# Kernel tuning notes

Hardware: AMD Instinct MI355X
Metric: run time of the kernel (lower is better)

Reference implementation:

```python
import jax, jax.numpy as jnp
import numpy as np

N_USERS, N_MOVIES, N_EDGES = 100000, 20000, 1000000
IN_UNITS, NUM_CLASSES = 128, 5


def _xavier(key, shape):
    # torch xavier_uniform_ on a Linear weight [out, in]; we store transposed [in, out]
    fan_in, fan_out = shape[0], shape[1]
    a = jnp.sqrt(6.0 / (fan_in + fan_out))
    return jax.random.uniform(key, shape, dtype=jnp.float32, minval=-a, maxval=a)


def setup_inputs() -> dict:
    key = jax.random.key(0)
    k1, k2, k3, k4, k5, k6, k7 = jax.random.split(key, 7)
    ufeat = jax.random.normal(k1, (N_USERS, IN_UNITS), dtype=jnp.float32)
    ifeat = jax.random.normal(k2, (N_MOVIES, IN_UNITS), dtype=jnp.float32)
    src_idx = jax.random.randint(k3, (N_EDGES,), 0, N_USERS, dtype=jnp.int32)
    dst_idx = jax.random.randint(k4, (N_EDGES,), 0, N_MOVIES, dtype=jnp.int32)
    W1 = _xavier(k5, (2 * IN_UNITS, IN_UNITS))   # Linear(2*in_units -> in_units)
    W2 = _xavier(k6, (IN_UNITS, IN_UNITS))       # Linear(in_units -> in_units)
    Wp = _xavier(k7, (IN_UNITS, NUM_CLASSES))    # predictor Linear(in_units -> num_classes)
    return {"ufeat": ufeat, "ifeat": ifeat, "src_idx": src_idx, "dst_idx": dst_idx,
            "W1": W1, "W2": W2, "Wp": Wp}


def reference(ufeat, ifeat, W1, W2, Wp, src_idx, dst_idx):
    # gather per-edge src/dst node features
    h_u = ufeat[src_idx]                 # [E, D]
    h_v = ifeat[dst_idx]                 # [E, D]
    h = jnp.concatenate([h_u, h_v], axis=1)          # [E, 2D]
    h = jax.nn.gelu(h @ W1, approximate=False)        # [E, D] (torch GELU default = exact erf)
    h = h @ W2                                        # [E, D]
    score = h @ Wp                                    # [E, C]
    return jnp.squeeze(score)
```

## Files before the change

kernel.cpp:

```cpp
#include <hip/hip_runtime.h>
#include <hip/hip_bf16.h>

#define D 128

typedef short bf16x8 __attribute__((ext_vector_type(8)));
typedef float f32x4 __attribute__((ext_vector_type(4)));
typedef float f32x2 __attribute__((ext_vector_type(2)));

__device__ __forceinline__ unsigned short f2bf(float x) {
    __hip_bfloat16 h = __float2bfloat16(x);
    return *reinterpret_cast<unsigned short*>(&h);
}
__device__ __forceinline__ float bflo(unsigned int w) { return __uint_as_float(w << 16); }
__device__ __forceinline__ float bfhi(unsigned int w) { return __uint_as_float(w & 0xffff0000u); }

__device__ __forceinline__ f32x2 gelu2(f32x2 z) {
    f32x2 z2 = z * z;
    f32x2 c1 = {0.1029466f, 0.1029466f};
    f32x2 c0 = {2.3022646f, 2.3022646f};
    f32x2 xe = z * __builtin_elementwise_fma(z2, c1, c0);
    f32x2 q;
    q.x = __builtin_amdgcn_exp2f(xe.x);
    q.y = __builtin_amdgcn_exp2f(xe.y);
    f32x2 d = q + 1.0f;
    f32x2 r;
    r.x = __builtin_amdgcn_rcpf(d.x);
    r.y = __builtin_amdgcn_rcpf(d.y);
    return __builtin_elementwise_fma(-z, r, z);
}

__device__ __forceinline__ float gelu_erf(float z) {
    float y = fabsf(z) * 0.70710678118654752f;
    float t = __builtin_amdgcn_rcpf(1.0f + 0.3275911f * y);
    float poly = ((((1.061405429f * t - 1.453152027f) * t + 1.421413741f) * t
                   - 0.284496736f) * t + 0.254829592f) * t;
    float e = __expf(-y * y);
    float erfv = 1.0f - poly * e;
    erfv = copysignf(erfv, z);
    return 0.5f * z * (1.0f + erfv);
}

__device__ __forceinline__ void node_body(const float* __restrict__ feat,
                                          const float* __restrict__ W1,
                                          int base_k, int Nn, int blk,
                                          unsigned short* __restrict__ outbf) {
    __shared__ unsigned short sB[128 * 136];
    const int t = threadIdx.x;
    const int r0 = blk * 64;

    #pragma unroll
    for (int i = 0; i < 16; ++i) {
        int f = (i * 256 + t) * 4;
        int k = f >> 7, j = f & 127;
        float4 v = *reinterpret_cast<const float4*>(&W1[(size_t)(base_k + k) * D + j]);
        sB[(j + 0) * 136 + k] = f2bf(v.x);
        sB[(j + 1) * 136 + k] = f2bf(v.y);
        sB[(j + 2) * 136 + k] = f2bf(v.z);
        sB[(j + 3) * 136 + k] = f2bf(v.w);
    }
    __syncthreads();

    const int wid = t >> 6, l = t & 63;
    const int m16 = l & 15, g4 = l >> 4;
    const int arow = r0 + wid * 16 + m16;
    const bool rok = arow < Nn;
    const float* rp = feat + (size_t)(rok ? arow : 0) * D;

    f32x4 acc[8];
    #pragma unroll
    for (int n = 0; n < 8; ++n) acc[n] = (f32x4){0.f, 0.f, 0.f, 0.f};

    #pragma unroll
    for (int kk = 0; kk < 4; ++kk) {
        int k0 = kk * 32 + g4 * 8;
        float4 f0 = make_float4(0.f, 0.f, 0.f, 0.f), f1 = f0;
        if (rok) {
            f0 = *reinterpret_cast<const float4*>(rp + k0);
            f1 = *reinterpret_cast<const float4*>(rp + k0 + 4);
        }
        union { bf16x8 v; unsigned short u[8]; } a;
        a.u[0] = f2bf(f0.x); a.u[1] = f2bf(f0.y); a.u[2] = f2bf(f0.z); a.u[3] = f2bf(f0.w);
        a.u[4] = f2bf(f1.x); a.u[5] = f2bf(f1.y); a.u[6] = f2bf(f1.z); a.u[7] = f2bf(f1.w);
        #pragma unroll
        for (int n = 0; n < 8; ++n) {
            bf16x8 b = *reinterpret_cast<const bf16x8*>(&sB[(n * 16 + m16) * 136 + k0]);
            acc[n] = __builtin_amdgcn_mfma_f32_16x16x32_bf16(a.v, b, acc[n], 0, 0, 0);
        }
    }
    #pragma unroll
    for (int n = 0; n < 8; ++n) {
        #pragma unroll
        for (int r = 0; r < 4; ++r) {
            int row = r0 + wid * 16 + g4 * 4 + r;
            if (row < Nn) outbf[(size_t)row * D + n * 16 + m16] = f2bf(acc[n][r]);
        }
    }
}

__global__ __launch_bounds__(256) void prep_kernel(const float* __restrict__ uf,
                                                   const float* __restrict__ vf,
                                                   const float* __restrict__ W1,
                                                   const float* __restrict__ W2,
                                                   const float* __restrict__ Wp,
                                                   int NU, int NM, int nbU, int nbM,
                                                   unsigned short* __restrict__ Abf,
                                                   unsigned short* __restrict__ Bbf,
                                                   unsigned short* __restrict__ Wcbf) {
    int b = blockIdx.x;
    if (b < nbU) {
        node_body(uf, W1, 0, NU, b, Abf);
    } else if (b < nbU + nbM) {
        node_body(vf, W1, D, NM, b - nbU, Bbf);
    } else {
        int t = threadIdx.x;
        #pragma unroll
        for (int i = 0; i < 8; ++i) {
            int idx = i * 256 + t;
            int col = idx >> 7, k = idx & 127;
            float acc = 0.f;
            if (col < 5) {
                #pragma unroll 8
                for (int j = 0; j < D; ++j) acc += W2[k * D + j] * Wp[j * 5 + col];
            }
            Wcbf[col * D + k] = f2bf(acc);
        }
    }
}

__global__ __launch_bounds__(256, 4) void edge_kernel(const unsigned short* __restrict__ A,
                                                      const unsigned short* __restrict__ B,
                                                      const int* __restrict__ src,
                                                      const int* __restrict__ dst,
                                                      const unsigned short* __restrict__ Wcbf,
                                                      float* __restrict__ out, int E) {
    const int l    = threadIdx.x & 63;
    const int er   = l & 15;
    const int quad = l >> 4;
    const int wid  = blockIdx.x * 4 + (threadIdx.x >> 6);
    const int nw   = gridDim.x * 4;

    bf16x8 wfrag[4];
    #pragma unroll
    for (int kk = 0; kk < 4; ++kk)
        wfrag[kk] = *reinterpret_cast<const bf16x8*>(&Wcbf[er * D + kk * 32 + quad * 8]);

    const int P = (E + 31) >> 5;
    if (wid >= P) return;
    const int Emax = E - 1;

    int ia = wid * 32 + er, ib = ia + 16;
    int sa = src[min(ia, Emax)], da = dst[min(ia, Emax)];
    int sb = src[min(ib, Emax)], db = dst[min(ib, Emax)];

    for (int p = wid; p < P; p += nw) {
        int pn = p + nw;
        int pc = pn < P ? pn : p;
        int ja = pc * 32 + er, jb = ja + 16;
        int san = src[min(ja, Emax)], dan = dst[min(ja, Emax)];
        int sbn = src[min(jb, Emax)], dbn = dst[min(jb, Emax)];

        const unsigned short* apA = A + ((size_t)sa << 7) + quad * 8;
        const unsigned short* bpA = B + ((size_t)da << 7) + quad * 8;
        const unsigned short* apB = A + ((size_t)sb << 7) + quad * 8;
        const unsigned short* bpB = B + ((size_t)db << 7) + quad * 8;
        uint4 a0[4], b0[4], a1[4], b1[4];
        #pragma unroll
        for (int kk = 0; kk < 4; ++kk) {
            a0[kk] = *reinterpret_cast<const uint4*>(apA + kk * 32);
            b0[kk] = *reinterpret_cast<const uint4*>(bpA + kk * 32);
            a1[kk] = *reinterpret_cast<const uint4*>(apB + kk * 32);
            b1[kk] = *reinterpret_cast<const uint4*>(bpB + kk * 32);
        }

        f32x4 accA = (f32x4){0.f, 0.f, 0.f, 0.f};
        f32x4 accB = accA;
        #pragma unroll
        for (int kk = 0; kk < 4; ++kk) {
            unsigned int aw[4] = {a0[kk].x, a0[kk].y, a0[kk].z, a0[kk].w};
            unsigned int bw[4] = {b0[kk].x, b0[kk].y, b0[kk].z, b0[kk].w};
            union { bf16x8 v; unsigned short u[8]; } frag;
            #pragma unroll
            for (int pp = 0; pp < 4; ++pp) {
                f32x2 za = {bflo(aw[pp]), bfhi(aw[pp])};
                f32x2 zb = {bflo(bw[pp]), bfhi(bw[pp])};
                f32x2 g = gelu2(za + zb);
                frag.u[2 * pp]     = f2bf(g.x);
                frag.u[2 * pp + 1] = f2bf(g.y);
            }
            accA = __builtin_amdgcn_mfma_f32_16x16x32_bf16(frag.v, wfrag[kk], accA, 0, 0, 0);
        }
        #pragma unroll
        for (int kk = 0; kk < 4; ++kk) {
            unsigned int aw[4] = {a1[kk].x, a1[kk].y, a1[kk].z, a1[kk].w};
            unsigned int bw[4] = {b1[kk].x, b1[kk].y, b1[kk].z, b1[kk].w};
            union { bf16x8 v; unsigned short u[8]; } frag;
            #pragma unroll
            for (int pp = 0; pp < 4; ++pp) {
                f32x2 za = {bflo(aw[pp]), bfhi(aw[pp])};
                f32x2 zb = {bflo(bw[pp]), bfhi(bw[pp])};
                f32x2 g = gelu2(za + zb);
                frag.u[2 * pp]     = f2bf(g.x);
                frag.u[2 * pp + 1] = f2bf(g.y);
            }
            accB = __builtin_amdgcn_mfma_f32_16x16x32_bf16(frag.v, wfrag[kk], accB, 0, 0, 0);
        }

        int e0 = p << 5;
        #pragma unroll
        for (int r = 0; r < 4; ++r) {
            int eA = e0 + quad * 4 + r;
            if (er < 5 && eA < E) out[(size_t)eA * 5 + er] = accA[r];
        }
        #pragma unroll
        for (int r = 0; r < 4; ++r) {
            int eB = e0 + 16 + quad * 4 + r;
            if (er < 5 && eB < E) out[(size_t)eB * 5 + er] = accB[r];
        }
        sa = san; da = dan; sb = sbn; db = dbn;
    }
}

__global__ __launch_bounds__(256) void fused_fallback(const float* __restrict__ uf,
                                                      const float* __restrict__ vf,
                                                      const int* __restrict__ src,
                                                      const int* __restrict__ dst,
                                                      const float* __restrict__ W1,
                                                      const float* __restrict__ W2,
                                                      const float* __restrict__ Wp,
                                                      float* __restrict__ out, int E) {
    __shared__ unsigned short sW[256 * 128];
    __shared__ float sWc[5 * 128];
    __shared__ float sH[4][256];
    const int t = threadIdx.x;
    #pragma unroll
    for (int i = 0; i < 32; ++i) {
        int f = (i * 256 + t) * 4;
        float4 v = *reinterpret_cast<const float4*>(&W1[f]);
        sW[f + 0] = f2bf(v.x); sW[f + 1] = f2bf(v.y);
        sW[f + 2] = f2bf(v.z); sW[f + 3] = f2bf(v.w);
    }
    for (int idx = t; idx < 640; idx += 256) {
        int c = idx >> 7, k = idx & 127;
        float a = 0.f;
        for (int m = 0; m < 128; ++m) a += W2[k * 128 + m] * Wp[m * 5 + c];
        sWc[c * 128 + k] = a;
    }
    __syncthreads();
    const int wid = t >> 6, l = t & 63;
    const int nw = gridDim.x * 4;
    for (int e = blockIdx.x * 4 + wid; e < E; e += nw) {
        int s = src[e], d0 = dst[e];
        float2 hu = *reinterpret_cast<const float2*>(&uf[(size_t)s * 128 + 2 * l]);
        float2 hv = *reinterpret_cast<const float2*>(&vf[(size_t)d0 * 128 + 2 * l]);
        sH[wid][2 * l] = hu.x; sH[wid][2 * l + 1] = hu.y;
        sH[wid][128 + 2 * l] = hv.x; sH[wid][128 + 2 * l + 1] = hv.y;
        __builtin_amdgcn_wave_barrier();
        float z0 = 0.f, z1 = 0.f;
        for (int k = 0; k < 256; ++k) {
            float h = sH[wid][k];
            z0 += h * __uint_as_float((unsigned int)sW[k * 128 + l] << 16);
            z1 += h * __uint_as_float((unsigned int)sW[k * 128 + l + 64] << 16);
        }
        float g0 = gelu_erf(z0), g1 = gelu_erf(z1);
        float acc[5];
        #pragma unroll
        for (int c = 0; c < 5; ++c)
            acc[c] = g0 * sWc[c * 128 + l] + g1 * sWc[c * 128 + l + 64];
        #pragma unroll
        for (int c = 0; c < 5; ++c) {
            float v = acc[c];
            v += __shfl_xor(v, 1);  v += __shfl_xor(v, 2);
            v += __shfl_xor(v, 4);  v += __shfl_xor(v, 8);
            v += __shfl_xor(v, 16); v += __shfl_xor(v, 32);
            acc[c] = v;
        }
        float v = acc[0];
        if (l == 1) v = acc[1];
        if (l == 2) v = acc[2];
        if (l == 3) v = acc[3];
        if (l == 4) v = acc[4];
        if (l < 5) out[(size_t)e * 5 + l] = v;
        __builtin_amdgcn_wave_barrier();
    }
}

extern "C" void kernel_launch(void* const* d_in, const int* in_sizes, int n_in,
                              void* d_out, int out_size, void* d_ws, size_t ws_size,
                              hipStream_t stream) {
    const float* ufeat = (const float*)d_in[0];
    const float* ifeat = (const float*)d_in[1];
    const int*   src   = (const int*)d_in[2];
    const int*   dst   = (const int*)d_in[3];
    const float* W1    = (const float*)d_in[4];
    const float* W2    = (const float*)d_in[5];
    const float* Wp    = (const float*)d_in[6];
    float* out = (float*)d_out;

    const int NU = in_sizes[0] / D;
    const int NM = in_sizes[1] / D;
    const int E  = in_sizes[2];

    size_t off_A = 4096;
    size_t szA = (size_t)NU * D * 2;
    size_t off_B = off_A + ((szA + 255) / 256) * 256;
    size_t need = off_B + (size_t)NM * D * 2;

    if (ws_size >= need) {
        unsigned short* Wcbf = (unsigned short*)d_ws;
        unsigned short* Abf  = (unsigned short*)((char*)d_ws + off_A);
        unsigned short* Bbf  = (unsigned short*)((char*)d_ws + off_B);
        int nbU = (NU + 63) / 64, nbM = (NM + 63) / 64;
        prep_kernel<<<dim3(nbU + nbM + 1), dim3(256), 0, stream>>>(
            ufeat, ifeat, W1, W2, Wp, NU, NM, nbU, nbM, Abf, Bbf, Wcbf);
        int P = (E + 31) >> 5;
        int blocks = (P + 3) / 4; if (blocks > 2048) blocks = 2048;
        edge_kernel<<<dim3(blocks), dim3(256), 0, stream>>>(Abf, Bbf, src, dst, Wcbf, out, E);
    } else {
        fused_fallback<<<dim3(4096), dim3(256), 0, stream>>>(ufeat, ifeat, src, dst,
                                                             W1, W2, Wp, out, E);
    }
}
```

Baseline: 113.9 us.

## Bucket-sort edges by source node and add pre-swizzled W1 node GEMM

Adds a counting sort of edges by src>>6 (histogram, scan, scatter) so the edge kernel gathers user rows with locality and can assign blocks per XCD. It also pre-transposes W1 into MFMA fragment order once, so the node GEMM uses 256-row tiles with a direct shared-memory copy. The aim is less random HBM/L2 traffic on the large A gather. The cost is four extra launches, a memset, atomics, a scattered output write through eid, and extra workspace traffic for the sd/eid buffers.

```diff
diff --git a/kernel.cpp b/kernel.cpp
--- a/kernel.cpp
+++ b/kernel.cpp
@@ -40,79 +40,25 @@
     return 0.5f * z * (1.0f + erfv);
 }
 
-__device__ __forceinline__ void node_body(const float* __restrict__ feat,
-                                          const float* __restrict__ W1,
-                                          int base_k, int Nn, int blk,
-                                          unsigned short* __restrict__ outbf) {
-    __shared__ unsigned short sB[128 * 136];
-    const int t = threadIdx.x;
-    const int r0 = blk * 64;
-
-    #pragma unroll
-    for (int i = 0; i < 16; ++i) {
-        int f = (i * 256 + t) * 4;
-        int k = f >> 7, j = f & 127;
-        float4 v = *reinterpret_cast<const float4*>(&W1[(size_t)(base_k + k) * D + j]);
-        sB[(j + 0) * 136 + k] = f2bf(v.x);
-        sB[(j + 1) * 136 + k] = f2bf(v.y);
-        sB[(j + 2) * 136 + k] = f2bf(v.z);
-        sB[(j + 3) * 136 + k] = f2bf(v.w);
-    }
-    __syncthreads();
-
-    const int wid = t >> 6, l = t & 63;
-    const int m16 = l & 15, g4 = l >> 4;
-    const int arow = r0 + wid * 16 + m16;
-    const bool rok = arow < Nn;
-    const float* rp = feat + (size_t)(rok ? arow : 0) * D;
-
-    f32x4 acc[8];
-    #pragma unroll
-    for (int n = 0; n < 8; ++n) acc[n] = (f32x4){0.f, 0.f, 0.f, 0.f};
-
-    #pragma unroll
-    for (int kk = 0; kk < 4; ++kk) {
-        int k0 = kk * 32 + g4 * 8;
-        float4 f0 = make_float4(0.f, 0.f, 0.f, 0.f), f1 = f0;
-        if (rok) {
-            f0 = *reinterpret_cast<const float4*>(rp + k0);
-            f1 = *reinterpret_cast<const float4*>(rp + k0 + 4);
-        }
-        union { bf16x8 v; unsigned short u[8]; } a;
-        a.u[0] = f2bf(f0.x); a.u[1] = f2bf(f0.y); a.u[2] = f2bf(f0.z); a.u[3] = f2bf(f0.w);
-        a.u[4] = f2bf(f1.x); a.u[5] = f2bf(f1.y); a.u[6] = f2bf(f1.z); a.u[7] = f2bf(f1.w);
-        #pragma unroll
-        for (int n = 0; n < 8; ++n) {
-            bf16x8 b = *reinterpret_cast<const bf16x8*>(&sB[(n * 16 + m16) * 136 + k0]);
-            acc[n] = __builtin_amdgcn_mfma_f32_16x16x32_bf16(a.v, b, acc[n], 0, 0, 0);
-        }
-    }
-    #pragma unroll
-    for (int n = 0; n < 8; ++n) {
-        #pragma unroll
-        for (int r = 0; r < 4; ++r) {
-            int row = r0 + wid * 16 + g4 * 4 + r;
-            if (row < Nn) outbf[(size_t)row * D + n * 16 + m16] = f2bf(acc[n][r]);
-        }
-    }
-}
-
-__global__ __launch_bounds__(256) void prep_kernel(const float* __restrict__ uf,
-                                                   const float* __restrict__ vf,
-                                                   const float* __restrict__ W1,
-                                                   const float* __restrict__ W2,
-                                                   const float* __restrict__ Wp,
-                                                   int NU, int NM, int nbU, int nbM,
-                                                   unsigned short* __restrict__ Abf,
-                                                   unsigned short* __restrict__ Bbf,
-                                                   unsigned short* __restrict__ Wcbf) {
-    int b = blockIdx.x;
-    if (b < nbU) {
-        node_body(uf, W1, 0, NU, b, Abf);
-    } else if (b < nbU + nbM) {
-        node_body(vf, W1, D, NM, b - nbU, Bbf);
+__global__ __launch_bounds__(256) void prep0_kernel(const float* __restrict__ W1,
+                                                    const float* __restrict__ W2,
+                                                    const float* __restrict__ Wp,
+                                                    unsigned short* __restrict__ W1T,
+                                                    unsigned short* __restrict__ Wcbf) {
+    const int b = blockIdx.x, t = threadIdx.x;
+    if (b < 64) {
+        int o0 = b * 1024 + t * 4;
+        unsigned short v[4];
+        #pragma unroll
+        for (int jj = 0; jj < 4; ++jj) {
+            int o = o0 + jj;
+            int j = o & 7, l = (o >> 3) & 63, kk = (o >> 9) & 3, n = (o >> 11) & 7, h = o >> 14;
+            int row = h * 128 + kk * 32 + (l >> 4) * 8 + j;
+            int col = n * 16 + (l & 15);
+            v[jj] = f2bf(W1[(size_t)row * D + col]);
+        }
+        *reinterpret_cast<ushort4*>(&W1T[o0]) = make_ushort4(v[0], v[1], v[2], v[3]);
     } else {
-        int t = threadIdx.x;
         #pragma unroll
         for (int i = 0; i < 8; ++i) {
             int idx = i * 256 + t;
@@ -127,12 +73,208 @@
     }
 }
 
-__global__ __launch_bounds__(256, 4) void edge_kernel(const unsigned short* __restrict__ A,
-                                                      const unsigned short* __restrict__ B,
-                                                      const int* __restrict__ src,
+__global__ __launch_bounds__(512) void node_kernel(const float* __restrict__ uf,
+                                                   const float* __restrict__ vf,
+                                                   const unsigned short* __restrict__ W1T,
+                                                   int NU, int NM, int nbU,
+                                                   unsigned short* __restrict__ Abf,
+                                                   unsigned short* __restrict__ Bbf) {
+    __shared__ unsigned short sW[16384];
+    const int b = blockIdx.x, t = threadIdx.x;
+
+    const float* feat;
+    unsigned short* outp;
+    int Nn, tile, h;
+    if (b < nbU) { feat = uf; outp = Abf; Nn = NU; tile = b;       h = 0; }
+    else         { feat = vf; outp = Bbf; Nn = NM; tile = b - nbU; h = 1; }
+    const int r0 = tile * 256;
+
+    {
+        const uint4* srcp = reinterpret_cast<const uint4*>(W1T + (size_t)h * 16384);
+        uint4* dstp = reinterpret_cast<uint4*>(sW);
+        #pragma unroll
+        for (int i = 0; i < 4; ++i) dstp[i * 512 + t] = srcp[i * 512 + t];
+    }
+    __syncthreads();
+
+    const int wv = t >> 6, l = t & 63;
+    const int m16 = l & 15, g4 = l >> 4;
+
+    #pragma unroll
+    for (int t16 = 0; t16 < 2; ++t16) {
+        const int rowbase = r0 + wv * 32 + t16 * 16;
+        if (rowbase >= Nn) break;
+        const int arow = rowbase + m16;
+        const bool rok = arow < Nn;
+        const float* rp = feat + (size_t)(rok ? arow : 0) * D;
+
+        union { bf16x8 v; unsigned short u[8]; } afr[4];
+        #pragma unroll
+        for (int kk = 0; kk < 4; ++kk) {
+            int k0 = kk * 32 + g4 * 8;
+            float4 f0 = make_float4(0.f, 0.f, 0.f, 0.f), f1 = f0;
+            if (rok) {
+                f0 = *reinterpret_cast<const float4*>(rp + k0);
+                f1 = *reinterpret_cast<const float4*>(rp + k0 + 4);
+            }
+            afr[kk].u[0] = f2bf(f0.x); afr[kk].u[1] = f2bf(f0.y);
+            afr[kk].u[2] = f2bf(f0.z); afr[kk].u[3] = f2bf(f0.w);
+            afr[kk].u[4] = f2bf(f1.x); afr[kk].u[5] = f2bf(f1.y);
+            afr[kk].u[6] = f2bf(f1.z); afr[kk].u[7] = f2bf(f1.w);
+        }
+
+        #pragma unroll
+        for (int n = 0; n < 8; ++n) {
+            f32x4 acc = (f32x4){0.f, 0.f, 0.f, 0.f};
+            #pragma unroll
+            for (int kk = 0; kk < 4; ++kk) {
+                bf16x8 bfr = *reinterpret_cast<const bf16x8*>(&sW[((n * 4 + kk) * 64 + l) * 8]);
+                acc = __builtin_amdgcn_mfma_f32_16x16x32_bf16(afr[kk].v, bfr, acc, 0, 0, 0);
+            }
+            #pragma unroll
+            for (int r = 0; r < 4; ++r) {
+                int row = rowbase + g4 * 4 + r;
+                if (row < Nn) outp[(size_t)row * D + n * 16 + m16] = f2bf(acc[r]);
+            }
+        }
+    }
+}
+
+__global__ __launch_bounds__(256) void hist_kernel(const int* __restrict__ src, int E, int NB,
+                                                   int* __restrict__ hist) {
+    __shared__ int lh[2048];
+    for (int i = threadIdx.x; i < NB; i += 256) lh[i] = 0;
+    __syncthreads();
+    for (int e = blockIdx.x * 256 + threadIdx.x; e < E; e += gridDim.x * 256)
+        atomicAdd(&lh[src[e] >> 6], 1);
+    __syncthreads();
+    for (int i = threadIdx.x; i < NB; i += 256) {
+        int v = lh[i];
+        if (v) atomicAdd(&hist[i], v);
+    }
+}
+
+__global__ __launch_bounds__(256) void scan_kernel(const int* __restrict__ hist, int NB,
+                                                   int* __restrict__ cursor) {
+    __shared__ int ps[256];
+    const int t = threadIdx.x;
+    int loc[8];
+    int tot = 0;
+    #pragma unroll
+    for (int i = 0; i < 8; ++i) {
+        int idx = t * 8 + i;
+        loc[i] = (idx < NB) ? hist[idx] : 0;
+        tot += loc[i];
+    }
+    ps[t] = tot;
+    __syncthreads();
+    for (int off = 1; off < 256; off <<= 1) {
+        int v = (t >= off) ? ps[t - off] : 0;
+        __syncthreads();
+        ps[t] += v;
+        __syncthreads();
+    }
+    int exc = ps[t] - tot;
+    #pragma unroll
+    for (int i = 0; i < 8; ++i) {
+        int idx = t * 8 + i;
+        if (idx < NB) cursor[idx] = exc;
+        exc += loc[i];
+    }
+}
+
+__global__ __launch_bounds__(256) void scatter_kernel(const int* __restrict__ src,
                                                       const int* __restrict__ dst,
-                                                      const unsigned short* __restrict__ Wcbf,
-                                                      float* __restrict__ out, int E) {
+                                                      int E, int* __restrict__ cursor,
+                                                      uint2* __restrict__ sd,
+                                                      int* __restrict__ eid) {
+    for (int e = blockIdx.x * 256 + threadIdx.x; e < E; e += gridDim.x * 256) {
+        int s = src[e];
+        int pos = atomicAdd(&cursor[s >> 6], 1);
+        sd[pos] = make_uint2((unsigned)s, (unsigned)dst[e]);
+        eid[pos] = e;
+    }
+}
+
+#define EITERS 8
+__global__ __launch_bounds__(256) void edge_sorted(const unsigned short* __restrict__ A,
+                                                   const unsigned short* __restrict__ B,
+                                                   const uint2* __restrict__ sd,
+                                                   const int* __restrict__ eid,
+                                                   const unsigned short* __restrict__ Wcbf,
+                                                   float* __restrict__ out, int E, int G) {
+    const int l    = threadIdx.x & 63;
+    const int er   = l & 15;
+    const int quad = l >> 4;
+
+    const int nb = gridDim.x;
+    const int qb = nb >> 3, rb = nb & 7;
+    const int xcd = blockIdx.x & 7, ib = blockIdx.x >> 3;
+    const int sb = (xcd < rb) ? xcd * (qb + 1) + ib : rb * (qb + 1) + (xcd - rb) * qb + ib;
+    const int wid = sb * 4 + (threadIdx.x >> 6);
+
+    bf16x8 wfrag[4];
+    #pragma unroll
+    for (int kk = 0; kk < 4; ++kk)
+        wfrag[kk] = *reinterpret_cast<const bf16x8*>(&Wcbf[er * D + kk * 32 + quad * 8]);
+
+    #pragma unroll 1
+    for (int it = 0; it < EITERS; ++it) {
+        int g = wid * EITERS + it;
+        if (g >= G) break;
+        int i16 = g << 4;
+
+        uint2 sdv = sd[min(i16 + er, E - 1)];
+        const unsigned short* ap = A + ((size_t)sdv.x << 7) + quad * 8;
+        const unsigned short* bp = B + ((size_t)sdv.y << 7) + quad * 8;
+        uint4 av[4], bv[4];
+        #pragma unroll
+        for (int kk = 0; kk < 4; ++kk) {
+            av[kk] = *reinterpret_cast<const uint4*>(ap + kk * 32);
+            bv[kk] = *reinterpret_cast<const uint4*>(bp + kk * 32);
+        }
+
+        int eb = i16 + quad * 4;
+        int evr[4];
+        if (i16 + 16 <= E) {
+            int4 ev = *reinterpret_cast<const int4*>(&eid[eb]);
+            evr[0] = ev.x; evr[1] = ev.y; evr[2] = ev.z; evr[3] = ev.w;
+        } else {
+            #pragma unroll
+            for (int r = 0; r < 4; ++r) evr[r] = eid[min(eb + r, E - 1)];
+        }
+
+        f32x4 acc = (f32x4){0.f, 0.f, 0.f, 0.f};
+        #pragma unroll
+        for (int kk = 0; kk < 4; ++kk) {
+            unsigned int aw[4] = {av[kk].x, av[kk].y, av[kk].z, av[kk].w};
+            unsigned int bw[4] = {bv[kk].x, bv[kk].y, bv[kk].z, bv[kk].w};
+            union { bf16x8 v; unsigned short u[8]; } frag;
+            #pragma unroll
+            for (int pp = 0; pp < 4; ++pp) {
+                f32x2 za = {bflo(aw[pp]), bfhi(aw[pp])};
+                f32x2 zb = {bflo(bw[pp]), bfhi(bw[pp])};
+                f32x2 gl = gelu2(za + zb);
+                frag.u[2 * pp]     = f2bf(gl.x);
+                frag.u[2 * pp + 1] = f2bf(gl.y);
+            }
+            acc = __builtin_amdgcn_mfma_f32_16x16x32_bf16(frag.v, wfrag[kk], acc, 0, 0, 0);
+        }
+
+        #pragma unroll
+        for (int r = 0; r < 4; ++r) {
+            int e = i16 + quad * 4 + r;
+            if (er < 5 && e < E) out[(size_t)evr[r] * 5 + er] = acc[r];
+        }
+    }
+}
+
+__global__ __launch_bounds__(256, 4) void edge_unsorted(const unsigned short* __restrict__ A,
+                                                        const unsigned short* __restrict__ B,
+                                                        const int* __restrict__ src,
+                                                        const int* __restrict__ dst,
+                                                        const unsigned short* __restrict__ Wcbf,
+                                                        float* __restrict__ out, int E) {
     const int l    = threadIdx.x & 63;
     const int er   = l & 15;
     const int quad = l >> 4;
@@ -299,22 +441,49 @@
     const int NU = in_sizes[0] / D;
     const int NM = in_sizes[1] / D;
     const int E  = in_sizes[2];
-
-    size_t off_A = 4096;
-    size_t szA = (size_t)NU * D * 2;
-    size_t off_B = off_A + ((szA + 255) / 256) * 256;
-    size_t need = off_B + (size_t)NM * D * 2;
-
-    if (ws_size >= need) {
-        unsigned short* Wcbf = (unsigned short*)d_ws;
+    const int NB = (NU + 63) >> 6;
+
+    size_t cur = 0;
+    auto alloc = [&](size_t bytes) { size_t o = cur; cur = (cur + bytes + 255) & ~(size_t)255; return o; };
+    size_t off_Wc   = alloc(4096);
+    size_t off_W1T  = alloc(65536);
+    size_t off_A    = alloc((size_t)NU * D * 2);
+    size_t off_B    = alloc((size_t)NM * D * 2);
+    size_t need_mid = cur;
+    size_t off_hist = alloc(2048 * 4);
+    size_t off_cur  = alloc(2048 * 4);
+    size_t off_sd   = alloc((size_t)E * 8);
+    size_t off_eid  = alloc((size_t)E * 4);
+    size_t need_full = cur;
+
+    if (ws_size >= need_mid) {
+        unsigned short* Wcbf = (unsigned short*)((char*)d_ws + off_Wc);
+        unsigned short* W1T  = (unsigned short*)((char*)d_ws + off_W1T);
         unsigned short* Abf  = (unsigned short*)((char*)d_ws + off_A);
         unsigned short* Bbf  = (unsigned short*)((char*)d_ws + off_B);
-        int nbU = (NU + 63) / 64, nbM = (NM + 63) / 64;
-        prep_kernel<<<dim3(nbU + nbM + 1), dim3(256), 0, stream>>>(
-            ufeat, ifeat, W1, W2, Wp, NU, NM, nbU, nbM, Abf, Bbf, Wcbf);
-        int P = (E + 31) >> 5;
-        int blocks = (P + 3) / 4; if (blocks > 2048) blocks = 2048;
-        edge_kernel<<<dim3(blocks), dim3(256), 0, stream>>>(Abf, Bbf, src, dst, Wcbf, out, E);
+
+        prep0_kernel<<<dim3(65), dim3(256), 0, stream>>>(W1, W2, Wp, W1T, Wcbf);
+        int nbU = (NU + 255) / 256, nbM = (NM + 255) / 256;
+        node_kernel<<<dim3(nbU + nbM), dim3(512), 0, stream>>>(ufeat, ifeat, W1T, NU, NM, nbU, Abf, Bbf);
+
+        if (ws_size >= need_full && NB <= 2048) {
+            int*   hist = (int*)((char*)d_ws + off_hist);
+            int*   curs = (int*)((char*)d_ws + off_cur);
+            uint2* sd   = (uint2*)((char*)d_ws + off_sd);
+            int*   eid  = (int*)((char*)d_ws + off_eid);
+
+            hipMemsetAsync(hist, 0, (size_t)NB * 4, stream);
+            hist_kernel<<<dim3(256), dim3(256), 0, stream>>>(src, E, NB, hist);
+            scan_kernel<<<dim3(1), dim3(256), 0, stream>>>(hist, NB, curs);
+            scatter_kernel<<<dim3(512), dim3(256), 0, stream>>>(src, dst, E, curs, sd, eid);
+
+            int G = (E + 15) >> 4;
+            int NWv = (G + EITERS - 1) / EITERS;
+            int blocks = (NWv + 3) / 4;
+            edge_sorted<<<dim3(blocks), dim3(256), 0, stream>>>(Abf, Bbf, sd, eid, Wcbf, out, E, G);
+        } else {
+            edge_unsorted<<<dim3(2048), dim3(256), 0, stream>>>(Abf, Bbf, src, dst, Wcbf, out, E);
+        }
     } else {
         fused_fallback<<<dim3(4096), dim3(256), 0, stream>>>(ufeat, ifeat, src, dst,
                                                              W1, W2, Wp, out, E);
```

Result: slower. 279.8 us (+145.7%).
